# Optimization experiments

Measured on AMD Instinct MI355X. Metric: run time of the kernel, lower is better.

Reference implementation:

```python
import jax, jax.numpy as jnp
import numpy as np

B, S, E, H = 8, 1024, 1024, 16
D = E // H  # head_dim = 64


def setup_inputs() -> dict:
    key = jax.random.key(0)
    ks = jax.random.split(key, 8)
    scale = 1.0 / np.sqrt(E)
    return {
        "query": jax.random.normal(ks[0], (B, S, E), jnp.float32),
        "key": jax.random.normal(ks[1], (B, S, E), jnp.float32),
        "value": jax.random.normal(ks[2], (B, S, E), jnp.float32),
        "q_w": jax.random.normal(ks[3], (E, E), jnp.float32) * scale,
        "q_b": jnp.zeros((E,), jnp.float32),
        "k_w": jax.random.normal(ks[4], (E, E), jnp.float32) * scale,
        "k_b": jnp.zeros((E,), jnp.float32),
        "v_w": jax.random.normal(ks[5], (E, E), jnp.float32) * scale,
        "v_b": jnp.zeros((E,), jnp.float32),
        "out_w": jax.random.normal(ks[6], (E, E), jnp.float32) * scale,
        "out_b": jnp.zeros((E,), jnp.float32),
    }


def reference(query, key, value, q_w, q_b, k_w, k_b, v_w, v_b, out_w, out_b):
    b = query.shape[0]
    scaling = 1.0 / jnp.sqrt(jnp.asarray(D, query.dtype))
    # torch Linear: x @ W.T + b; split heads -> (b, H, S, D)
    def proj(x, w, bias):
        y = jnp.einsum('bse,fe->bsf', x, w) + bias
        return y.reshape(b, -1, H, D).transpose(0, 2, 1, 3)
    q = proj(query, q_w, q_b)
    k = proj(key, k_w, k_b)
    v = proj(value, v_w, v_b)
    scores = jnp.einsum('bhqd,bhkd->bhqk', q, k) * scaling
    attn_weights = jax.nn.softmax(scores, axis=-1)
    # dropout is identity in eval mode (deterministic reference)
    context = jnp.einsum('bhqk,bhkd->bhqd', attn_weights, v)
    context = context.transpose(0, 2, 1, 3).reshape(b, -1, E)
    output = jnp.einsum('bse,fe->bsf', context, out_w) + out_b
    return (attn_weights, output)
```

## Files before the change

kernel.cpp:

```cpp
#include <hip/hip_runtime.h>

typedef __attribute__((ext_vector_type(8))) short short8;
typedef __attribute__((ext_vector_type(4))) float f32x4;
typedef unsigned short u16;

#define DEVI __device__ __forceinline__

DEVI u16 f2bf(float f) {
  unsigned u = __float_as_uint(f);
  unsigned r = (u + 0x7fffu + ((u >> 16) & 1u)) >> 16;
  return (u16)r;
}

DEVI void gl2lds16(const void* g, void* l) {
  __builtin_amdgcn_global_load_lds((const __attribute__((address_space(1))) void*)g,
                                   (__attribute__((address_space(3))) void*)l, 16, 0, 0);
}

template<int ROWS, int BKE>
DEVI void stage_bf16(const u16* __restrict__ g, int ld, u16* lds, int tid) {
  constexpr int CPR = BKE / 8;
  constexpr int CH  = ROWS * CPR;
  const int wave = tid >> 6, lane = tid & 63;
#pragma unroll
  for (int i = 0; i < CH / 256; i++) {
    int c = (i * 4 + wave) * 64 + lane;
    int row = c / CPR;
    int colb = (c % CPR) * 16;
    gl2lds16((const char*)g + (long)row * ld * 2 + colb, (char*)lds + (long)c * 16);
  }
}

template<int FM, int FN, int BKE>
DEVI void kstep(const u16* Alds, const u16* Blds, int lane, int wr, int wc, int kk,
                f32x4 (*acc)[FN]) {
  const int ro = lane & 15, ko = kk + (lane >> 4) * 8;
  short8 a[FM], b[FN];
#pragma unroll
  for (int m = 0; m < FM; m++) a[m] = *(const short8*)(Alds + (wr + m * 16 + ro) * BKE + ko);
#pragma unroll
  for (int n = 0; n < FN; n++) b[n] = *(const short8*)(Blds + (wc + n * 16 + ro) * BKE + ko);
#pragma unroll
  for (int m = 0; m < FM; m++)
#pragma unroll
    for (int n = 0; n < FN; n++)
      acc[m][n] = __builtin_amdgcn_mfma_f32_16x16x32_bf16(a[m], b[n], acc[m][n], 0, 0, 0);
}

struct CvtArgs {
  const float* s[7];
  u16* d[7];
  int n8[7];
};

__global__ __launch_bounds__(256) void cvt_all(CvtArgs a) {
  const int t = blockIdx.y;
  const int n = a.n8[t];
  const float* __restrict__ s = a.s[t];
  u16* __restrict__ d = a.d[t];
  for (long i = blockIdx.x * 256 + threadIdx.x; i < n; i += (long)gridDim.x * 256) {
    float4 v0 = ((const float4*)s)[2 * i];
    float4 v1 = ((const float4*)s)[2 * i + 1];
    ushort4 h0, h1;
    h0.x = f2bf(v0.x); h0.y = f2bf(v0.y); h0.z = f2bf(v0.z); h0.w = f2bf(v0.w);
    h1.x = f2bf(v1.x); h1.y = f2bf(v1.y); h1.z = f2bf(v1.z); h1.w = f2bf(v1.w);
    ((ushort4*)d)[2 * i] = h0;
    ((ushort4*)d)[2 * i + 1] = h1;
  }
}

struct Biases { const float* p[3]; };

__global__ __launch_bounds__(256) void proj3_kernel(const u16* __restrict__ Xb,
                                                    const u16* __restrict__ Wb,
                                                    Biases bs,
                                                    u16* __restrict__ Outb) {
  __shared__ u16 Alds[128 * 64];
  __shared__ u16 Blds[128 * 64];
  const int tid = threadIdx.x, lane = tid & 63, w = tid >> 6;
  const int wr = (w >> 1) * 64, wc = (w & 1) * 64;
  const int z = blockIdx.z;
  const u16* X = Xb + (long)z * 8388608;
  const u16* W = Wb + (long)z * 1048576;
  const float* bias = bs.p[z];
  u16* Out = Outb + (long)z * 8388608;
  const long rowB = (long)blockIdx.x * 128;
  const int colB = blockIdx.y * 128;
  f32x4 acc[4][4] = {};
  for (int k0 = 0; k0 < 1024; k0 += 64) {
    stage_bf16<128, 64>(X + rowB * 1024 + k0, 1024, Alds, tid);
    stage_bf16<128, 64>(W + (long)colB * 1024 + k0, 1024, Blds, tid);
    __syncthreads();
    kstep<4, 4, 64>(Alds, Blds, lane, wr, wc, 0, acc);
    kstep<4, 4, 64>(Alds, Blds, lane, wr, wc, 32, acc);
    __syncthreads();
  }
  const int ro = (lane >> 4) * 4, co = lane & 15;
  const float sc = (z == 0) ? 0.125f : 1.0f;
  if (z < 2) {
#pragma unroll
    for (int n = 0; n < 4; n++) {
      const int col = colB + wc + n * 16 + co;
      const float bv = bias[col];
      const int h = col >> 6, d = col & 63;
#pragma unroll
      for (int m = 0; m < 4; m++)
#pragma unroll
        for (int j = 0; j < 4; j++) {
          long r = rowB + wr + m * 16 + ro + j;
          long bq = r >> 10, s = r & 1023;
          Out[(((bq * 16 + h) * 1024 + s) << 6) + d] = f2bf((acc[m][n][j] + bv) * sc);
        }
    }
  } else {
#pragma unroll
    for (int n = 0; n < 4; n++) {
      const int col = colB + wc + n * 16 + co;
      const float bv = bias[col];
      const long h = col >> 6, d = col & 63;
#pragma unroll
      for (int m = 0; m < 4; m++) {
        long r0 = rowB + wr + m * 16 + ro;
        long bq = r0 >> 10, s = r0 & 1023;
        ushort4 pk;
        pk.x = f2bf(acc[m][n][0] + bv);
        pk.y = f2bf(acc[m][n][1] + bv);
        pk.z = f2bf(acc[m][n][2] + bv);
        pk.w = f2bf(acc[m][n][3] + bv);
        *(ushort4*)(Out + (((bq * 16 + h) << 16) | (d << 10) | s)) = pk;
      }
    }
  }
}

__global__ __launch_bounds__(256) void flash_kernel(const u16* __restrict__ Q,
                                                    const u16* __restrict__ K,
                                                    const u16* __restrict__ Vt,
                                                    float* __restrict__ attn,
                                                    u16* __restrict__ Ctx) {
  __shared__ u16 lds[24576];
  u16* const Pl = lds + 16384;
  const int tid = threadIdx.x, lane = tid & 63, w = tid >> 6;
  const int z = blockIdx.x;
  const int rowB = blockIdx.y * 128;
  const int b = z >> 4, h = z & 15;
  const u16* Qb  = Q  + (long)z * 65536 + (long)rowB * 64;
  const u16* Kb  = K  + (long)z * 65536;
  const u16* Vtb = Vt + (long)z * 65536;
  const int ro = lane & 15, ko8 = (lane >> 4) * 8;
  const int qw = w * 32;

  short8 aq[2][2];
#pragma unroll
  for (int m = 0; m < 2; m++)
#pragma unroll
    for (int kt = 0; kt < 2; kt++)
      aq[m][kt] = *(const short8*)(Qb + (qw + m * 16 + ro) * 64 + kt * 32 + ko8);

  float lsum[8];
#pragma unroll
  for (int i = 0; i < 8; i++) lsum[i] = 0.0f;

  stage_bf16<128, 64>(Kb, 64, lds, tid);
  __syncthreads();
  for (int kb = 0; kb < 8; kb++) {
    const int cur = kb & 1;
    if (kb < 7) stage_bf16<128, 64>(Kb + (kb + 1) * 8192, 64, lds + ((kb + 1) & 1) * 8192, tid);
    const u16* Kc = lds + cur * 8192;
    f32x4 acc[2][8] = {};
#pragma unroll
    for (int kt = 0; kt < 2; kt++) {
      short8 bfr[8];
#pragma unroll
      for (int n = 0; n < 8; n++)
        bfr[n] = *(const short8*)(Kc + (n * 16 + ro) * 64 + kt * 32 + ko8);
#pragma unroll
      for (int m = 0; m < 2; m++)
#pragma unroll
        for (int n = 0; n < 8; n++)
          acc[m][n] = __builtin_amdgcn_mfma_f32_16x16x32_bf16(aq[m][kt], bfr[n], acc[m][n], 0, 0, 0);
    }
#pragma unroll
    for (int m = 0; m < 2; m++)
#pragma unroll
      for (int j = 0; j < 4; j++) {
        const int i = m * 4 + j;
        float e0 = __expf(acc[m][0][j]) + __expf(acc[m][1][j]) +
                   __expf(acc[m][2][j]) + __expf(acc[m][3][j]);
        float e1 = __expf(acc[m][4][j]) + __expf(acc[m][5][j]) +
                   __expf(acc[m][6][j]) + __expf(acc[m][7][j]);
        lsum[i] += e0 + e1;
      }
    __syncthreads();
  }
  float linv[8];
#pragma unroll
  for (int i = 0; i < 8; i++) {
    float s = lsum[i];
#pragma unroll
    for (int o = 8; o > 0; o >>= 1) s += __shfl_xor(s, o, 64);
    linv[i] = 1.0f / s;
  }
  __syncthreads();

  f32x4 acc_o[2][4] = {};
  float* ab = attn + ((long)z << 20) + (long)rowB * 1024;
  stage_bf16<64, 64>(Kb, 64, lds, tid);
  stage_bf16<64, 64>(Vtb, 1024, lds + 8192, tid);
  __syncthreads();
  for (int kb = 0; kb < 16; kb++) {
    const int cur = kb & 1, nxt = cur ^ 1;
    if (kb < 15) {
      stage_bf16<64, 64>(Kb + (kb + 1) * 4096, 64, lds + nxt * 4096, tid);
      stage_bf16<64, 64>(Vtb + (kb + 1) * 64, 1024, lds + 8192 + nxt * 4096, tid);
    }
    const u16* Kc = lds + cur * 4096;
    const u16* Vc = lds + 8192 + cur * 4096;
    f32x4 acc[2][4] = {};
#pragma unroll
    for (int kt = 0; kt < 2; kt++) {
      short8 bfr[4];
#pragma unroll
      for (int n = 0; n < 4; n++)
        bfr[n] = *(const short8*)(Kc + (n * 16 + ro) * 64 + kt * 32 + ko8);
#pragma unroll
      for (int m = 0; m < 2; m++)
#pragma unroll
        for (int n = 0; n < 4; n++)
          acc[m][n] = __builtin_amdgcn_mfma_f32_16x16x32_bf16(aq[m][kt], bfr[n], acc[m][n], 0, 0, 0);
    }
#pragma unroll
    for (int m = 0; m < 2; m++)
#pragma unroll
      for (int j = 0; j < 4; j++) {
        const int i = m * 4 + j;
        const int ql = qw + m * 16 + (lane >> 4) * 4 + j;
        float* rowp = ab + (long)ql * 1024 + kb * 64;
        u16* prow = Pl + ql * 64;
        const int sw = ((ql & 7) << 3);
#pragma unroll
        for (int n = 0; n < 4; n++) {
          const int col = n * 16 + (lane & 15);
          float p = __expf(acc[m][n][j]) * linv[i];
          __builtin_nontemporal_store(p, rowp + col);
          prow[col ^ sw] = f2bf(p);
        }
      }
    asm volatile("s_waitcnt lgkmcnt(0)" ::: "memory");
    __builtin_amdgcn_sched_barrier(0);
#pragma unroll
    for (int kt = 0; kt < 2; kt++) {
      short8 pa[2], bv[4];
#pragma unroll
      for (int m = 0; m < 2; m++) {
        const int row = qw + m * 16 + ro;
        pa[m] = *(const short8*)(Pl + row * 64 + ((kt * 32 + ko8) ^ ((row & 7) << 3)));
      }
#pragma unroll
      for (int n = 0; n < 4; n++)
        bv[n] = *(const short8*)(Vc + (n * 16 + ro) * 64 + kt * 32 + ko8);
#pragma unroll
      for (int m = 0; m < 2; m++)
#pragma unroll
        for (int n = 0; n < 4; n++)
          acc_o[m][n] = __builtin_amdgcn_mfma_f32_16x16x32_bf16(pa[m], bv[n], acc_o[m][n], 0, 0, 0);
    }
    __syncthreads();
  }

  u16* cb = Ctx + ((long)b << 20) + (long)h * 64;
#pragma unroll
  for (int m = 0; m < 2; m++)
#pragma unroll
    for (int j = 0; j < 4; j++) {
      const long s = rowB + qw + m * 16 + (lane >> 4) * 4 + j;
#pragma unroll
      for (int n = 0; n < 4; n++)
        cb[s * 1024 + n * 16 + (lane & 15)] = f2bf(acc_o[m][n][j]);
    }
}

__global__ __launch_bounds__(256) void outb_kernel(const u16* __restrict__ Ctx,
                                                   const u16* __restrict__ W,
                                                   const float* __restrict__ bias,
                                                   float* __restrict__ Out) {
  __shared__ u16 Alds[128 * 64];
  __shared__ u16 Blds[128 * 64];
  const int tid = threadIdx.x, lane = tid & 63, w = tid >> 6;
  const int wr = (w >> 1) * 64, wc = (w & 1) * 64;
  const long rowB = (long)blockIdx.x * 128;
  const int colB = blockIdx.y * 128;
  f32x4 acc[4][4] = {};
  for (int k0 = 0; k0 < 1024; k0 += 64) {
    stage_bf16<128, 64>(Ctx + rowB * 1024 + k0, 1024, Alds, tid);
    stage_bf16<128, 64>(W + (long)colB * 1024 + k0, 1024, Blds, tid);
    __syncthreads();
    kstep<4, 4, 64>(Alds, Blds, lane, wr, wc, 0, acc);
    kstep<4, 4, 64>(Alds, Blds, lane, wr, wc, 32, acc);
    __syncthreads();
  }
  const int ro = (lane >> 4) * 4, co = lane & 15;
#pragma unroll
  for (int n = 0; n < 4; n++) {
    const int col = colB + wc + n * 16 + co;
    const float bv = bias[col];
#pragma unroll
    for (int m = 0; m < 4; m++)
#pragma unroll
      for (int j = 0; j < 4; j++) {
        long r = rowB + wr + m * 16 + ro + j;
        __builtin_nontemporal_store(acc[m][n][j] + bv, Out + r * 1024 + col);
      }
  }
}

extern "C" void kernel_launch(void* const* d_in, const int* in_sizes, int n_in,
                              void* d_out, int out_size, void* d_ws, size_t ws_size,
                              hipStream_t stream) {
  const float* query = (const float*)d_in[0];
  const float* key   = (const float*)d_in[1];
  const float* value = (const float*)d_in[2];
  const float* q_w   = (const float*)d_in[3];
  const float* q_b   = (const float*)d_in[4];
  const float* k_w   = (const float*)d_in[5];
  const float* k_b   = (const float*)d_in[6];
  const float* v_w   = (const float*)d_in[7];
  const float* v_b   = (const float*)d_in[8];
  const float* out_w = (const float*)d_in[9];
  const float* out_b = (const float*)d_in[10];

  const long MB = 1048576L;
  char* ws = (char*)d_ws;
  u16* Qp  = (u16*)(ws);
  u16* Kp  = (u16*)(ws + 16 * MB);
  u16* Vt  = (u16*)(ws + 32 * MB);
  u16* Qb  = (u16*)(ws + 48 * MB);
  u16* Kb  = (u16*)(ws + 64 * MB);
  u16* Vb  = (u16*)(ws + 80 * MB);
  u16* Ctx = (u16*)(ws + 64 * MB);
  u16* Wq  = (u16*)(ws + 96 * MB);
  u16* Wk  = (u16*)(ws + 98 * MB);
  u16* Wv  = (u16*)(ws + 100 * MB);
  u16* Wo  = (u16*)(ws + 102 * MB);

  float* attn = (float*)d_out;
  float* outp = (float*)d_out + 134217728L;

  CvtArgs ca;
  ca.s[0] = query; ca.d[0] = Qb; ca.n8[0] = 1048576;
  ca.s[1] = key;   ca.d[1] = Kb; ca.n8[1] = 1048576;
  ca.s[2] = value; ca.d[2] = Vb; ca.n8[2] = 1048576;
  ca.s[3] = q_w;   ca.d[3] = Wq; ca.n8[3] = 131072;
  ca.s[4] = k_w;   ca.d[4] = Wk; ca.n8[4] = 131072;
  ca.s[5] = v_w;   ca.d[5] = Wv; ca.n8[5] = 131072;
  ca.s[6] = out_w; ca.d[6] = Wo; ca.n8[6] = 131072;

  Biases bs;
  bs.p[0] = q_b; bs.p[1] = k_b; bs.p[2] = v_b;

  dim3 blk(256);
  cvt_all<<<dim3(2048, 7), blk, 0, stream>>>(ca);
  proj3_kernel<<<dim3(64, 8, 3), blk, 0, stream>>>(Qb, Wq, bs, Qp);
  flash_kernel<<<dim3(128, 8), blk, 0, stream>>>(Qp, Kp, Vt, attn, Ctx);
  outb_kernel<<<dim3(64, 8), blk, 0, stream>>>(Ctx, Wo, out_b, outp);
}
```

Measured before the change: 337.8 us.

## Fuse fp32-to-bf16 conversion into GEMM staging and widen flash blocks to 512 threads

Drops the separate conversion kernel. The projection and output GEMMs now load fp32 inputs and weights directly, convert them to bf16 in registers, and write padded LDS tiles (stride 72). This removes one launch and a full write-then-read of the bf16 copies, but gives up the async global-to-LDS loads in those GEMMs and re-converts each weight tile once per row block. The flash kernel now runs 512 threads covering 256 query rows per block, and the first K/V tile for the second pass is issued before the row-sum reduction.

```diff
diff --git a/kernel.cpp b/kernel.cpp
--- a/kernel.cpp
+++ b/kernel.cpp
@@ -17,29 +17,45 @@
                                    (__attribute__((address_space(3))) void*)l, 16, 0, 0);
 }
 
-template<int ROWS, int BKE>
+template<int ROWS, int BKE, int NT>
 DEVI void stage_bf16(const u16* __restrict__ g, int ld, u16* lds, int tid) {
   constexpr int CPR = BKE / 8;
   constexpr int CH  = ROWS * CPR;
+  constexpr int NW  = NT / 64;
   const int wave = tid >> 6, lane = tid & 63;
 #pragma unroll
-  for (int i = 0; i < CH / 256; i++) {
-    int c = (i * 4 + wave) * 64 + lane;
+  for (int i = 0; i < CH / NT; i++) {
+    int c = (i * NW + wave) * 64 + lane;
     int row = c / CPR;
     int colb = (c % CPR) * 16;
     gl2lds16((const char*)g + (long)row * ld * 2 + colb, (char*)lds + (long)c * 16);
   }
 }
 
-template<int FM, int FN, int BKE>
+template<int ROWS, int BKE, int LD>
+DEVI void stage_f32(const float* __restrict__ g, int ld, u16* lds, int tid) {
+  constexpr int QPR = BKE / 4;
+  constexpr int Q4 = ROWS * QPR;
+#pragma unroll
+  for (int i = 0; i < Q4 / 256; i++) {
+    int q = i * 256 + tid;
+    int row = q / QPR, c4 = q % QPR;
+    float4 v = *(const float4*)(g + (long)row * ld + c4 * 4);
+    ushort4 h;
+    h.x = f2bf(v.x); h.y = f2bf(v.y); h.z = f2bf(v.z); h.w = f2bf(v.w);
+    *(ushort4*)(lds + row * LD + c4 * 4) = h;
+  }
+}
+
+template<int FM, int FN, int LDA, int LDB>
 DEVI void kstep(const u16* Alds, const u16* Blds, int lane, int wr, int wc, int kk,
                 f32x4 (*acc)[FN]) {
   const int ro = lane & 15, ko = kk + (lane >> 4) * 8;
   short8 a[FM], b[FN];
 #pragma unroll
-  for (int m = 0; m < FM; m++) a[m] = *(const short8*)(Alds + (wr + m * 16 + ro) * BKE + ko);
-#pragma unroll
-  for (int n = 0; n < FN; n++) b[n] = *(const short8*)(Blds + (wc + n * 16 + ro) * BKE + ko);
+  for (int m = 0; m < FM; m++) a[m] = *(const short8*)(Alds + (wr + m * 16 + ro) * LDA + ko);
+#pragma unroll
+  for (int n = 0; n < FN; n++) b[n] = *(const short8*)(Blds + (wc + n * 16 + ro) * LDB + ko);
 #pragma unroll
   for (int m = 0; m < FM; m++)
 #pragma unroll
@@ -47,52 +63,27 @@
       acc[m][n] = __builtin_amdgcn_mfma_f32_16x16x32_bf16(a[m], b[n], acc[m][n], 0, 0, 0);
 }
 
-struct CvtArgs {
-  const float* s[7];
-  u16* d[7];
-  int n8[7];
-};
-
-__global__ __launch_bounds__(256) void cvt_all(CvtArgs a) {
-  const int t = blockIdx.y;
-  const int n = a.n8[t];
-  const float* __restrict__ s = a.s[t];
-  u16* __restrict__ d = a.d[t];
-  for (long i = blockIdx.x * 256 + threadIdx.x; i < n; i += (long)gridDim.x * 256) {
-    float4 v0 = ((const float4*)s)[2 * i];
-    float4 v1 = ((const float4*)s)[2 * i + 1];
-    ushort4 h0, h1;
-    h0.x = f2bf(v0.x); h0.y = f2bf(v0.y); h0.z = f2bf(v0.z); h0.w = f2bf(v0.w);
-    h1.x = f2bf(v1.x); h1.y = f2bf(v1.y); h1.z = f2bf(v1.z); h1.w = f2bf(v1.w);
-    ((ushort4*)d)[2 * i] = h0;
-    ((ushort4*)d)[2 * i + 1] = h1;
-  }
-}
-
-struct Biases { const float* p[3]; };
-
-__global__ __launch_bounds__(256) void proj3_kernel(const u16* __restrict__ Xb,
-                                                    const u16* __restrict__ Wb,
-                                                    Biases bs,
-                                                    u16* __restrict__ Outb) {
-  __shared__ u16 Alds[128 * 64];
-  __shared__ u16 Blds[128 * 64];
+struct Ptrs { const float* x[3]; const float* w[3]; const float* b[3]; };
+
+__global__ __launch_bounds__(256) void proj3_kernel(Ptrs ps, u16* __restrict__ Outb) {
+  __shared__ u16 Alds[128 * 72];
+  __shared__ u16 Blds[128 * 72];
   const int tid = threadIdx.x, lane = tid & 63, w = tid >> 6;
   const int wr = (w >> 1) * 64, wc = (w & 1) * 64;
   const int z = blockIdx.z;
-  const u16* X = Xb + (long)z * 8388608;
-  const u16* W = Wb + (long)z * 1048576;
-  const float* bias = bs.p[z];
+  const float* X = ps.x[z];
+  const float* W = ps.w[z];
+  const float* bias = ps.b[z];
   u16* Out = Outb + (long)z * 8388608;
   const long rowB = (long)blockIdx.x * 128;
   const int colB = blockIdx.y * 128;
   f32x4 acc[4][4] = {};
   for (int k0 = 0; k0 < 1024; k0 += 64) {
-    stage_bf16<128, 64>(X + rowB * 1024 + k0, 1024, Alds, tid);
-    stage_bf16<128, 64>(W + (long)colB * 1024 + k0, 1024, Blds, tid);
-    __syncthreads();
-    kstep<4, 4, 64>(Alds, Blds, lane, wr, wc, 0, acc);
-    kstep<4, 4, 64>(Alds, Blds, lane, wr, wc, 32, acc);
+    stage_f32<128, 64, 72>(X + rowB * 1024 + k0, 1024, Alds, tid);
+    stage_f32<128, 64, 72>(W + (long)colB * 1024 + k0, 1024, Blds, tid);
+    __syncthreads();
+    kstep<4, 4, 72, 72>(Alds, Blds, lane, wr, wc, 0, acc);
+    kstep<4, 4, 72, 72>(Alds, Blds, lane, wr, wc, 32, acc);
     __syncthreads();
   }
   const int ro = (lane >> 4) * 4, co = lane & 15;
@@ -133,16 +124,16 @@
   }
 }
 
-__global__ __launch_bounds__(256) void flash_kernel(const u16* __restrict__ Q,
+__global__ __launch_bounds__(512) void flash_kernel(const u16* __restrict__ Q,
                                                     const u16* __restrict__ K,
                                                     const u16* __restrict__ Vt,
                                                     float* __restrict__ attn,
                                                     u16* __restrict__ Ctx) {
-  __shared__ u16 lds[24576];
+  __shared__ u16 lds[32768];
   u16* const Pl = lds + 16384;
   const int tid = threadIdx.x, lane = tid & 63, w = tid >> 6;
   const int z = blockIdx.x;
-  const int rowB = blockIdx.y * 128;
+  const int rowB = blockIdx.y * 256;
   const int b = z >> 4, h = z & 15;
   const u16* Qb  = Q  + (long)z * 65536 + (long)rowB * 64;
   const u16* Kb  = K  + (long)z * 65536;
@@ -161,11 +152,11 @@
 #pragma unroll
   for (int i = 0; i < 8; i++) lsum[i] = 0.0f;
 
-  stage_bf16<128, 64>(Kb, 64, lds, tid);
+  stage_bf16<128, 64, 512>(Kb, 64, lds, tid);
   __syncthreads();
   for (int kb = 0; kb < 8; kb++) {
     const int cur = kb & 1;
-    if (kb < 7) stage_bf16<128, 64>(Kb + (kb + 1) * 8192, 64, lds + ((kb + 1) & 1) * 8192, tid);
+    if (kb < 7) stage_bf16<128, 64, 512>(Kb + (kb + 1) * 8192, 64, lds + ((kb + 1) & 1) * 8192, tid);
     const u16* Kc = lds + cur * 8192;
     f32x4 acc[2][8] = {};
 #pragma unroll
@@ -193,6 +184,9 @@
       }
     __syncthreads();
   }
+
+  stage_bf16<64, 64, 512>(Kb, 64, lds, tid);
+  stage_bf16<64, 64, 512>(Vtb, 1024, lds + 8192, tid);
   float linv[8];
 #pragma unroll
   for (int i = 0; i < 8; i++) {
@@ -205,14 +199,11 @@
 
   f32x4 acc_o[2][4] = {};
   float* ab = attn + ((long)z << 20) + (long)rowB * 1024;
-  stage_bf16<64, 64>(Kb, 64, lds, tid);
-  stage_bf16<64, 64>(Vtb, 1024, lds + 8192, tid);
-  __syncthreads();
   for (int kb = 0; kb < 16; kb++) {
     const int cur = kb & 1, nxt = cur ^ 1;
     if (kb < 15) {
-      stage_bf16<64, 64>(Kb + (kb + 1) * 4096, 64, lds + nxt * 4096, tid);
-      stage_bf16<64, 64>(Vtb + (kb + 1) * 64, 1024, lds + 8192 + nxt * 4096, tid);
+      stage_bf16<64, 64, 512>(Kb + (kb + 1) * 4096, 64, lds + nxt * 4096, tid);
+      stage_bf16<64, 64, 512>(Vtb + (kb + 1) * 64, 1024, lds + 8192 + nxt * 4096, tid);
     }
     const u16* Kc = lds + cur * 4096;
     const u16* Vc = lds + 8192 + cur * 4096;
@@ -281,22 +272,22 @@
 }
 
 __global__ __launch_bounds__(256) void outb_kernel(const u16* __restrict__ Ctx,
-                                                   const u16* __restrict__ W,
+                                                   const float* __restrict__ W,
                                                    const float* __restrict__ bias,
                                                    float* __restrict__ Out) {
   __shared__ u16 Alds[128 * 64];
-  __shared__ u16 Blds[128 * 64];
+  __shared__ u16 Blds[128 * 72];
   const int tid = threadIdx.x, lane = tid & 63, w = tid >> 6;
   const int wr = (w >> 1) * 64, wc = (w & 1) * 64;
   const long rowB = (long)blockIdx.x * 128;
   const int colB = blockIdx.y * 128;
   f32x4 acc[4][4] = {};
   for (int k0 = 0; k0 < 1024; k0 += 64) {
-    stage_bf16<128, 64>(Ctx + rowB * 1024 + k0, 1024, Alds, tid);
-    stage_bf16<128, 64>(W + (long)colB * 1024 + k0, 1024, Blds, tid);
-    __syncthreads();
-    kstep<4, 4, 64>(Alds, Blds, lane, wr, wc, 0, acc);
-    kstep<4, 4, 64>(Alds, Blds, lane, wr, wc, 32, acc);
+    stage_bf16<128, 64, 256>(Ctx + rowB * 1024 + k0, 1024, Alds, tid);
+    stage_f32<128, 64, 72>(W + (long)colB * 1024 + k0, 1024, Blds, tid);
+    __syncthreads();
+    kstep<4, 4, 64, 72>(Alds, Blds, lane, wr, wc, 0, acc);
+    kstep<4, 4, 64, 72>(Alds, Blds, lane, wr, wc, 32, acc);
     __syncthreads();
   }
   const int ro = (lane >> 4) * 4, co = lane & 15;
@@ -334,33 +325,17 @@
   u16* Qp  = (u16*)(ws);
   u16* Kp  = (u16*)(ws + 16 * MB);
   u16* Vt  = (u16*)(ws + 32 * MB);
-  u16* Qb  = (u16*)(ws + 48 * MB);
-  u16* Kb  = (u16*)(ws + 64 * MB);
-  u16* Vb  = (u16*)(ws + 80 * MB);
-  u16* Ctx = (u16*)(ws + 64 * MB);
-  u16* Wq  = (u16*)(ws + 96 * MB);
-  u16* Wk  = (u16*)(ws + 98 * MB);
-  u16* Wv  = (u16*)(ws + 100 * MB);
-  u16* Wo  = (u16*)(ws + 102 * MB);
+  u16* Ctx = (u16*)(ws + 48 * MB);
 
   float* attn = (float*)d_out;
   float* outp = (float*)d_out + 134217728L;
 
-  CvtArgs ca;
-  ca.s[0] = query; ca.d[0] = Qb; ca.n8[0] = 1048576;
-  ca.s[1] = key;   ca.d[1] = Kb; ca.n8[1] = 1048576;
-  ca.s[2] = value; ca.d[2] = Vb; ca.n8[2] = 1048576;
-  ca.s[3] = q_w;   ca.d[3] = Wq; ca.n8[3] = 131072;
-  ca.s[4] = k_w;   ca.d[4] = Wk; ca.n8[4] = 131072;
-  ca.s[5] = v_w;   ca.d[5] = Wv; ca.n8[5] = 131072;
-  ca.s[6] = out_w; ca.d[6] = Wo; ca.n8[6] = 131072;
-
-  Biases bs;
-  bs.p[0] = q_b; bs.p[1] = k_b; bs.p[2] = v_b;
-
-  dim3 blk(256);
-  cvt_all<<<dim3(2048, 7), blk, 0, stream>>>(ca);
-  proj3_kernel<<<dim3(64, 8, 3), blk, 0, stream>>>(Qb, Wq, bs, Qp);
-  flash_kernel<<<dim3(128, 8), blk, 0, stream>>>(Qp, Kp, Vt, attn, Ctx);
-  outb_kernel<<<dim3(64, 8), blk, 0, stream>>>(Ctx, Wo, out_b, outp);
-}
+  Ptrs ps;
+  ps.x[0] = query; ps.w[0] = q_w; ps.b[0] = q_b;
+  ps.x[1] = key;   ps.w[1] = k_w; ps.b[1] = k_b;
+  ps.x[2] = value; ps.w[2] = v_w; ps.b[2] = v_b;
+
+  proj3_kernel<<<dim3(64, 8, 3), dim3(256), 0, stream>>>(ps, Qp);
+  flash_kernel<<<dim3(128, 4), dim3(512), 0, stream>>>(Qp, Kp, Vt, attn, Ctx);
+  outb_kernel<<<dim3(64, 8), dim3(256), 0, stream>>>(Ctx, out_w, out_b, outp);
+}
```

After: 546.6 us. +61.8%, slower.
